# Kernel optimization log

Hardware: AMD Instinct MI355X
Metric: run time of the kernel (lower is better)

The kernel has to match this reference:

```python
import jax, jax.numpy as jnp
import numpy as np

TAU = 0.07          # softmax temperature
THR = 0.3           # Jaccard similarity threshold for positive pairs
EPS_NORM = 1e-12    # F.normalize eps


def setup_inputs() -> dict:
    key = jax.random.key(0)
    k1, k2, k3 = jax.random.split(key, 3)
    N, D, A = 4096, 128, 512
    z1 = jax.random.normal(k1, (N, D), dtype=jnp.float32)
    z2 = jax.random.normal(k2, (N, D), dtype=jnp.float32)
    labels = jax.random.randint(k3, (N, A), 0, 2).astype(jnp.int32)
    return {"z1": z1, "z2": z2, "labels": labels}


def _l2_normalize(x):
    n = jnp.linalg.norm(x, axis=-1, keepdims=True)
    return x / jnp.maximum(n, EPS_NORM)


def reference(z1, z2, labels):
    # Implements the N > 1000 (chunked) branch of SupConLoss.forward,
    # vectorized over all anchors at once (chunking is just tiling; math identical).
    N = z1.shape[0]
    idx = jnp.arange(N)

    z1n = _l2_normalize(z1)                       # (N, D)
    z2n = _l2_normalize(z2)                       # (N, D)
    z_all = jnp.concatenate([z1n, z2n], axis=0)   # (2N, D)

    # Jaccard label similarity -> positive-pair mask
    lab = labels.astype(jnp.float32)              # (N, A)
    inter = lab @ lab.T                           # (N, N)
    s = lab.sum(axis=1, keepdims=True)            # (N, 1)
    union = s + s.T - inter
    jaccard = inter / (union + 1e-8)
    pos_label = jaccard >= THR                    # (N, N) bool

    # pos mask over 2N columns: label-positives in both halves,
    # augmented view [j, N+j] forced True, self column [j, j] forced False.
    pos_mask = jnp.concatenate([pos_label, pos_label], axis=1)  # (N, 2N)
    pos_mask = pos_mask.at[idx, N + idx].set(True)
    pos_mask = pos_mask.at[idx, idx].set(False)

    # similarity of z1 anchors against all 2N embeddings
    sim = (z1n @ z_all.T) / TAU                   # (N, 2N)
    sim = sim - jax.lax.stop_gradient(sim.max(axis=1, keepdims=True))
    exp_sim = jnp.exp(sim)

    # denominator excludes the self column [j, j]
    denom = exp_sim.sum(axis=1, keepdims=True) - exp_sim[idx, idx][:, None]
    log_prob = sim - jnp.log(denom + 1e-8)

    num_pos = jnp.maximum(pos_mask.sum(axis=1), 1)
    loss_per_sample = -jnp.where(pos_mask, log_prob, 0.0).sum(axis=1) / num_pos
    return loss_per_sample.sum() / N
```

## Files before the change

kernel.cpp:

```cpp
#include <hip/hip_runtime.h>
#include <math.h>

#define N_ROWS 4096
#define DIM    128
#define A_LAB  512
#define INV_TAU 14.285714285714286f
#define C_EXP   20.609929155556620f

typedef __attribute__((ext_vector_type(8))) short short8;
typedef __attribute__((ext_vector_type(4))) float f32x4;
typedef __attribute__((ext_vector_type(4))) int i32x4;
typedef __attribute__((ext_vector_type(16))) int i32x16;


__device__ __forceinline__ unsigned short f2bf(float f) {
  unsigned int u = __builtin_bit_cast(unsigned int, f);
  u += 0x7fffu + ((u >> 16) & 1u);
  return (unsigned short)(u >> 16);
}

__global__ __launch_bounds__(256) void k_norm_pack(
    const float* __restrict__ z1, const float* __restrict__ z2,
    const int* __restrict__ labels,
    unsigned int* __restrict__ zbf, uint2* __restrict__ labs8,
    int* __restrict__ s, float* __restrict__ part, float* __restrict__ out)
{
  {
    const int idx = blockIdx.x * 256 + threadIdx.x;
    if (idx < 3 * 4096) part[idx] = 0.0f;
    if (idx == 0) out[0] = 0.0f;
  }
  const int wave = threadIdx.x >> 6, lane = threadIdx.x & 63;
  const int r = blockIdx.x * 4 + wave;
  const float* src = (r < N_ROWS) ? (z1 + (size_t)r * DIM)
                                  : (z2 + (size_t)(r - N_ROWS) * DIM);
  float2 x = ((const float2*)src)[lane];
  float ss = x.x * x.x + x.y * x.y;
  #pragma unroll
  for (int off = 32; off > 0; off >>= 1) ss += __shfl_xor(ss, off);
  const float inv = 1.0f / fmaxf(sqrtf(ss), 1e-12f);
  const unsigned int lo = f2bf(x.x * inv);
  const unsigned int hi = f2bf(x.y * inv);
  {
    const int u = lane >> 2, p = lane & 3;
    const int kf = u >> 2, quad = u & 3;
    const int g = r >> 4;
    zbf[(size_t)(((g * 4 + kf) * 64) + ((r & 15) + (quad << 4))) * 4 + p] = (hi << 16) | lo;
  }

  if (r < N_ROWS) {
    const int4* lp = (const int4*)(labels + (size_t)r * A_LAB);
    const int4 a = lp[2 * lane], b = lp[2 * lane + 1];
    const unsigned int w0 = (unsigned int)(a.x != 0)       | ((unsigned int)(a.y != 0) << 8)
                          | ((unsigned int)(a.z != 0) << 16) | ((unsigned int)(a.w != 0) << 24);
    const unsigned int w1 = (unsigned int)(b.x != 0)       | ((unsigned int)(b.y != 0) << 8)
                          | ((unsigned int)(b.z != 0) << 16) | ((unsigned int)(b.w != 0) << 24);
    uint2 v; v.x = w0; v.y = w1;
    const int ul = lane >> 1, hp = lane & 1;
    const int ks = ul >> 1, h = ul & 1;
    const int g = r >> 5;
    labs8[(size_t)(((g * 16 + ks) * 64) + ((r & 31) + (h << 5))) * 2 + hp] = v;
    int cnt = __popc(w0) + __popc(w1);
    #pragma unroll
    for (int off = 32; off > 0; off >>= 1) cnt += __shfl_xor(cnt, off);
    if (lane == 0) s[r] = cnt;
  }
}

__global__ __launch_bounds__(512, 2) void k_fused(
    const unsigned char* __restrict__ labs8, const int* __restrict__ s,
    const unsigned short* __restrict__ zbf, float* __restrict__ part)
{
  __shared__ unsigned int pmL[128 * 4];
  const int tid = threadIdx.x;
  const int ibase = blockIdx.x * 128, jbase = blockIdx.y * 128;
  const int wave = tid >> 6, lane = tid & 63;
  const bool diag = (ibase == jbase);
  const char* gl = (const char*)labs8;
  const char* gz = (const char*)zbf;

  const int jwr = (wave >> 2) * 64;
  const int jwc = (wave & 3) * 32;
  const int col32 = lane & 31, h = lane >> 5;

  const int s3i = 3 * s[ibase + jwr + lane];
  const int s3j = 3 * s[jbase + jwc + col32];

  i32x16 jacc[2];
  #pragma unroll
  for (int rt = 0; rt < 2; ++rt)
    #pragma unroll
    for (int e = 0; e < 16; ++e) jacc[rt][e] = 0;

  const int gI = (ibase + jwr) >> 5;
  const int gJ = (jbase + jwc) >> 5;
  #pragma unroll
  for (int batch = 0; batch < 2; ++batch) {
    i32x4 av[8][2], bv[8];
    #pragma unroll
    for (int k = 0; k < 8; ++k) {
      const int ks = batch * 8 + k;
      av[k][0] = *(const i32x4*)(gl + (size_t)((gI * 16 + ks) * 64 + lane) * 16);
      av[k][1] = *(const i32x4*)(gl + (size_t)(((gI + 1) * 16 + ks) * 64 + lane) * 16);
      bv[k]    = *(const i32x4*)(gl + (size_t)((gJ * 16 + ks) * 64 + lane) * 16);
    }
    #pragma unroll
    for (int k = 0; k < 8; ++k) {
      jacc[0] = __builtin_amdgcn_mfma_i32_32x32x32_i8(av[k][0], bv[k], jacc[0], 0, 0, 0);
      jacc[1] = __builtin_amdgcn_mfma_i32_32x32x32_i8(av[k][1], bv[k], jacc[1], 0, 0, 0);
    }
  }

  const int wl = wave & 3;
  #pragma unroll
  for (int rt = 0; rt < 2; ++rt)
    #pragma unroll
    for (int reg = 0; reg < 16; ++reg) {
      const int r0 = (reg & 3) + 8 * (reg >> 2);
      const int si = __shfl(s3i, rt * 32 + r0 + 4 * h);
      const bool pred = 13 * jacc[rt][reg] >= si + s3j;
      const unsigned long long bal = __ballot(pred);
      const int lr = jwr + rt * 32 + r0;
      if (lane == 0)      pmL[lr * 4 + wl]       = (unsigned int)bal;
      else if (lane == 1) pmL[(lr + 4) * 4 + wl] = (unsigned int)(bal >> 32);
    }

  const int col = lane & 15, quad = lane >> 4;
  const int srow = wave * 16;
  const int gA = (ibase + srow) >> 4;
  short8 afr[4];
  #pragma unroll
  for (int kf = 0; kf < 4; ++kf)
    afr[kf] = *(const short8*)(gz + (size_t)((gA * 4 + kf) * 64 + lane) * 16);

  __syncthreads();

  uint4 pw[4];
  #pragma unroll
  for (int reg = 0; reg < 4; ++reg)
    pw[reg] = *(const uint4*)&pmL[(srow + quad * 4 + reg) * 4];

  float lacc[4], Sacc[4], Pcnt[4];
  #pragma unroll
  for (int reg = 0; reg < 4; ++reg) { lacc[reg] = 0; Sacc[reg] = 0; Pcnt[reg] = 0; }

  #pragma unroll
  for (int half = 0; half < 2; ++half) {
    const int gB = ((half ? N_ROWS : 0) + jbase) >> 4;
    f32x4 acc[8];
    #pragma unroll
    for (int nt = 0; nt < 8; ++nt) acc[nt] = (f32x4){0, 0, 0, 0};

    #pragma unroll
    for (int batch = 0; batch < 2; ++batch) {
      short8 bv[4][4];
      #pragma unroll
      for (int q = 0; q < 4; ++q) {
        const int nt = batch * 4 + q;
        #pragma unroll
        for (int kf = 0; kf < 4; ++kf)
          bv[q][kf] = *(const short8*)(gz + (size_t)(((gB + nt) * 4 + kf) * 64 + lane) * 16);
      }
      #pragma unroll
      for (int q = 0; q < 4; ++q) {
        const int nt = batch * 4 + q;
        #pragma unroll
        for (int kf = 0; kf < 4; ++kf)
          acc[nt] = __builtin_amdgcn_mfma_f32_16x16x32_bf16(afr[kf], bv[q][kf], acc[nt], 0, 0, 0);
      }
    }

    if (!diag) {
      #pragma unroll
      for (int nt = 0; nt < 8; ++nt) {
        const int bitpos = (nt & 1) * 16 + col;
        #pragma unroll
        for (int reg = 0; reg < 4; ++reg) {
          const unsigned int w = ((const unsigned int*)&pw[reg])[nt >> 1];
          const float d = acc[nt][reg];
          lacc[reg] += exp2f(fmaf(d, C_EXP, -C_EXP));
          if ((w >> bitpos) & 1) Sacc[reg] += d;
        }
      }
    } else {
      const bool left = (half == 0);
      #pragma unroll
      for (int nt = 0; nt < 8; ++nt) {
        const int joff = nt * 16 + col;
        const int jc = jbase + joff;
        const int bitpos = joff & 31;
        #pragma unroll
        for (int reg = 0; reg < 4; ++reg) {
          const int i = ibase + srow + quad * 4 + reg;
          const unsigned int w = ((const unsigned int*)&pw[reg])[nt >> 1];
          const float d = acc[nt][reg];
          const bool bit = (w >> bitpos) & 1;
          const bool self = left && (jc == i);
          const bool pos = left ? (bit && !self) : (bit || (jc == i));
          const float e = exp2f(fmaf(d, C_EXP, -C_EXP));
          if (!self) lacc[reg] += e;
          if (pos) { Sacc[reg] += d; Pcnt[reg] += 1.0f; }
        }
      }
    }
  }

  #pragma unroll
  for (int reg = 0; reg < 4; ++reg) {
    float l = lacc[reg], S = Sacc[reg], P = Pcnt[reg];
    #pragma unroll
    for (int m = 1; m < 16; m <<= 1) {
      l += __shfl_xor(l, m);
      S += __shfl_xor(S, m);
      if (diag) P += __shfl_xor(P, m);
    }
    if (col == 0) {
      const int li = srow + quad * 4 + reg;
      const int i = ibase + li;
      if (!diag) {
        const uint4 w = pw[reg];
        P = 2.0f * (float)(__popc(w.x) + __popc(w.y) + __popc(w.z) + __popc(w.w));
      }
      atomicAdd(&part[i], l);
      atomicAdd(&part[4096 + i], S);
      atomicAdd(&part[8192 + i], P);
    }
  }
}

__global__ __launch_bounds__(128) void k_loss(
    const float* __restrict__ part, float* __restrict__ out)
{
  const int a = blockIdx.x * 128 + threadIdx.x;
  const float l = part[a];
  const float S = part[4096 + a];
  const float P = part[8192 + a];
  const float np = fmaxf(P, 1.0f);
  float v = INV_TAU + logf(l + 1e-8f) - (S * INV_TAU) / np;
  #pragma unroll
  for (int off = 32; off > 0; off >>= 1) v += __shfl_xor(v, off);
  __shared__ float ws2[2];
  const int wave = threadIdx.x >> 6, lane = threadIdx.x & 63;
  if (lane == 0) ws2[wave] = v;
  __syncthreads();
  if (threadIdx.x == 0) atomicAdd(out, (ws2[0] + ws2[1]) * (1.0f / (float)N_ROWS));
}

extern "C" void kernel_launch(void* const* d_in, const int* in_sizes, int n_in,
                              void* d_out, int out_size, void* d_ws, size_t ws_size,
                              hipStream_t stream) {
  const float* z1 = (const float*)d_in[0];
  const float* z2 = (const float*)d_in[1];
  const int* labels = (const int*)d_in[2];
  float* out = (float*)d_out;
  char* ws = (char*)d_ws;

  unsigned int* zbf    = (unsigned int*)(ws);
  uint2* labs8         = (uint2*)(ws + 2097152);
  int* s               = (int*)(ws + 4194304);
  float* part          = (float*)(ws + 4210688);

  hipLaunchKernelGGL(k_norm_pack, dim3(2048), dim3(256), 0, stream,
                     z1, z2, labels, zbf, labs8, s, part, out);
  hipLaunchKernelGGL(k_fused, dim3(32, 32), dim3(512), 0, stream,
                     (const unsigned char*)labs8, s, (const unsigned short*)zbf, part);
  hipLaunchKernelGGL(k_loss, dim3(32), dim3(128), 0, stream, part, out);
}
```

Before: 108.5 us.

## Exploit symmetry of label and z1 Gram matrices with upper-triangular block grid

The fused kernel now launches only the upper-triangular 528 blocks instead of the full 32x32 grid. The label Jaccard mask and the z1·z1 similarity block are computed once per off-diagonal pair and applied to both row i and row j through column-wise reductions. The z1·z2 tiles for both directions are still computed separately. This roughly halves the Jaccard popcount work and one GEMM half per pair, at the cost of more atomics, a triangular index decode loop, and per-block imbalance.

```diff
diff --git a/kernel.cpp b/kernel.cpp
--- a/kernel.cpp
+++ b/kernel.cpp
@@ -73,9 +73,12 @@
 {
   __shared__ unsigned int pmL[128 * 4];
   const int tid = threadIdx.x;
-  const int ibase = blockIdx.x * 128, jbase = blockIdx.y * 128;
+  int t = blockIdx.x, bi = 0;
+  while (t >= 32 - bi) { t -= 32 - bi; ++bi; }
+  const int bj = bi + t;
+  const int ibase = bi * 128, jbase = bj * 128;
   const int wave = tid >> 6, lane = tid & 63;
-  const bool diag = (ibase == jbase);
+  const bool diag = (bi == bj);
   const char* gl = (const char*)labs8;
   const char* gz = (const char*)zbf;
 
@@ -140,49 +143,35 @@
   for (int reg = 0; reg < 4; ++reg)
     pw[reg] = *(const uint4*)&pmL[(srow + quad * 4 + reg) * 4];
 
-  float lacc[4], Sacc[4], Pcnt[4];
-  #pragma unroll
-  for (int reg = 0; reg < 4; ++reg) { lacc[reg] = 0; Sacc[reg] = 0; Pcnt[reg] = 0; }
-
-  #pragma unroll
-  for (int half = 0; half < 2; ++half) {
-    const int gB = ((half ? N_ROWS : 0) + jbase) >> 4;
-    f32x4 acc[8];
-    #pragma unroll
-    for (int nt = 0; nt < 8; ++nt) acc[nt] = (f32x4){0, 0, 0, 0};
-
-    #pragma unroll
-    for (int batch = 0; batch < 2; ++batch) {
-      short8 bv[4][4];
-      #pragma unroll
-      for (int q = 0; q < 4; ++q) {
-        const int nt = batch * 4 + q;
-        #pragma unroll
-        for (int kf = 0; kf < 4; ++kf)
-          bv[q][kf] = *(const short8*)(gz + (size_t)(((gB + nt) * 4 + kf) * 64 + lane) * 16);
-      }
-      #pragma unroll
-      for (int q = 0; q < 4; ++q) {
-        const int nt = batch * 4 + q;
-        #pragma unroll
-        for (int kf = 0; kf < 4; ++kf)
-          acc[nt] = __builtin_amdgcn_mfma_f32_16x16x32_bf16(afr[kf], bv[q][kf], acc[nt], 0, 0, 0);
-      }
-    }
-
-    if (!diag) {
-      #pragma unroll
-      for (int nt = 0; nt < 8; ++nt) {
-        const int bitpos = (nt & 1) * 16 + col;
-        #pragma unroll
-        for (int reg = 0; reg < 4; ++reg) {
-          const unsigned int w = ((const unsigned int*)&pw[reg])[nt >> 1];
-          const float d = acc[nt][reg];
-          lacc[reg] += exp2f(fmaf(d, C_EXP, -C_EXP));
-          if ((w >> bitpos) & 1) Sacc[reg] += d;
-        }
-      }
-    } else {
+  if (diag) {
+    float lacc[4], Sacc[4], Pcnt[4];
+    #pragma unroll
+    for (int reg = 0; reg < 4; ++reg) { lacc[reg] = 0; Sacc[reg] = 0; Pcnt[reg] = 0; }
+
+    #pragma unroll
+    for (int half = 0; half < 2; ++half) {
+      const int gB = ((half ? N_ROWS : 0) + jbase) >> 4;
+      f32x4 acc[8];
+      #pragma unroll
+      for (int nt = 0; nt < 8; ++nt) acc[nt] = (f32x4){0, 0, 0, 0};
+      #pragma unroll
+      for (int batch = 0; batch < 2; ++batch) {
+        short8 bv[4][4];
+        #pragma unroll
+        for (int q = 0; q < 4; ++q) {
+          const int nt = batch * 4 + q;
+          #pragma unroll
+          for (int kf = 0; kf < 4; ++kf)
+            bv[q][kf] = *(const short8*)(gz + (size_t)(((gB + nt) * 4 + kf) * 64 + lane) * 16);
+        }
+        #pragma unroll
+        for (int q = 0; q < 4; ++q) {
+          const int nt = batch * 4 + q;
+          #pragma unroll
+          for (int kf = 0; kf < 4; ++kf)
+            acc[nt] = __builtin_amdgcn_mfma_f32_16x16x32_bf16(afr[kf], bv[q][kf], acc[nt], 0, 0, 0);
+        }
+      }
       const bool left = (half == 0);
       #pragma unroll
       for (int nt = 0; nt < 8; ++nt) {
@@ -203,27 +192,184 @@
         }
       }
     }
-  }
-
-  #pragma unroll
-  for (int reg = 0; reg < 4; ++reg) {
-    float l = lacc[reg], S = Sacc[reg], P = Pcnt[reg];
-    #pragma unroll
-    for (int m = 1; m < 16; m <<= 1) {
-      l += __shfl_xor(l, m);
-      S += __shfl_xor(S, m);
-      if (diag) P += __shfl_xor(P, m);
-    }
-    if (col == 0) {
-      const int li = srow + quad * 4 + reg;
-      const int i = ibase + li;
-      if (!diag) {
-        const uint4 w = pw[reg];
-        P = 2.0f * (float)(__popc(w.x) + __popc(w.y) + __popc(w.z) + __popc(w.w));
-      }
-      atomicAdd(&part[i], l);
-      atomicAdd(&part[4096 + i], S);
-      atomicAdd(&part[8192 + i], P);
+    #pragma unroll
+    for (int reg = 0; reg < 4; ++reg) {
+      float l = lacc[reg], S = Sacc[reg], P = Pcnt[reg];
+      #pragma unroll
+      for (int m = 1; m < 16; m <<= 1) {
+        l += __shfl_xor(l, m);
+        S += __shfl_xor(S, m);
+        P += __shfl_xor(P, m);
+      }
+      if (col == 0) {
+        const int i = ibase + srow + quad * 4 + reg;
+        atomicAdd(&part[i], l);
+        atomicAdd(&part[4096 + i], S);
+        atomicAdd(&part[8192 + i], P);
+      }
+    }
+  } else {
+    float lacc[4], Sacc[4];
+    #pragma unroll
+    for (int reg = 0; reg < 4; ++reg) { lacc[reg] = 0; Sacc[reg] = 0; }
+
+    {
+      const int gB = jbase >> 4;
+      f32x4 acc[8];
+      #pragma unroll
+      for (int nt = 0; nt < 8; ++nt) acc[nt] = (f32x4){0, 0, 0, 0};
+      #pragma unroll
+      for (int batch = 0; batch < 2; ++batch) {
+        short8 bv[4][4];
+        #pragma unroll
+        for (int q = 0; q < 4; ++q) {
+          const int nt = batch * 4 + q;
+          #pragma unroll
+          for (int kf = 0; kf < 4; ++kf)
+            bv[q][kf] = *(const short8*)(gz + (size_t)(((gB + nt) * 4 + kf) * 64 + lane) * 16);
+        }
+        #pragma unroll
+        for (int q = 0; q < 4; ++q) {
+          const int nt = batch * 4 + q;
+          #pragma unroll
+          for (int kf = 0; kf < 4; ++kf)
+            acc[nt] = __builtin_amdgcn_mfma_f32_16x16x32_bf16(afr[kf], bv[q][kf], acc[nt], 0, 0, 0);
+        }
+      }
+      float lc[8], Sc[8], Pc[8];
+      #pragma unroll
+      for (int nt = 0; nt < 8; ++nt) { lc[nt] = 0; Sc[nt] = 0; Pc[nt] = 0; }
+      #pragma unroll
+      for (int nt = 0; nt < 8; ++nt) {
+        const int bitpos = (nt & 1) * 16 + col;
+        #pragma unroll
+        for (int reg = 0; reg < 4; ++reg) {
+          const unsigned int w = ((const unsigned int*)&pw[reg])[nt >> 1];
+          const float d = acc[nt][reg];
+          const bool bit = (w >> bitpos) & 1;
+          const float e = exp2f(fmaf(d, C_EXP, -C_EXP));
+          lacc[reg] += e; lc[nt] += e;
+          if (bit) { Sacc[reg] += d; Sc[nt] += d; Pc[nt] += 1.0f; }
+        }
+      }
+      #pragma unroll
+      for (int nt = 0; nt < 8; ++nt) {
+        float l = lc[nt], S = Sc[nt], P = Pc[nt];
+        l += __shfl_xor(l, 16); l += __shfl_xor(l, 32);
+        S += __shfl_xor(S, 16); S += __shfl_xor(S, 32);
+        P += __shfl_xor(P, 16); P += __shfl_xor(P, 32);
+        if (quad == 0) {
+          const int j = jbase + nt * 16 + col;
+          atomicAdd(&part[j], l);
+          atomicAdd(&part[4096 + j], S);
+          atomicAdd(&part[8192 + j], 2.0f * P);
+        }
+      }
+    }
+
+    {
+      const int gB = (N_ROWS + jbase) >> 4;
+      f32x4 acc[8];
+      #pragma unroll
+      for (int nt = 0; nt < 8; ++nt) acc[nt] = (f32x4){0, 0, 0, 0};
+      #pragma unroll
+      for (int batch = 0; batch < 2; ++batch) {
+        short8 bv[4][4];
+        #pragma unroll
+        for (int q = 0; q < 4; ++q) {
+          const int nt = batch * 4 + q;
+          #pragma unroll
+          for (int kf = 0; kf < 4; ++kf)
+            bv[q][kf] = *(const short8*)(gz + (size_t)(((gB + nt) * 4 + kf) * 64 + lane) * 16);
+        }
+        #pragma unroll
+        for (int q = 0; q < 4; ++q) {
+          const int nt = batch * 4 + q;
+          #pragma unroll
+          for (int kf = 0; kf < 4; ++kf)
+            acc[nt] = __builtin_amdgcn_mfma_f32_16x16x32_bf16(afr[kf], bv[q][kf], acc[nt], 0, 0, 0);
+        }
+      }
+      #pragma unroll
+      for (int nt = 0; nt < 8; ++nt) {
+        const int bitpos = (nt & 1) * 16 + col;
+        #pragma unroll
+        for (int reg = 0; reg < 4; ++reg) {
+          const unsigned int w = ((const unsigned int*)&pw[reg])[nt >> 1];
+          const float d = acc[nt][reg];
+          lacc[reg] += exp2f(fmaf(d, C_EXP, -C_EXP));
+          if ((w >> bitpos) & 1) Sacc[reg] += d;
+        }
+      }
+      #pragma unroll
+      for (int reg = 0; reg < 4; ++reg) {
+        float l = lacc[reg], S = Sacc[reg];
+        #pragma unroll
+        for (int m = 1; m < 16; m <<= 1) { l += __shfl_xor(l, m); S += __shfl_xor(S, m); }
+        if (col == 0) {
+          const int i = ibase + srow + quad * 4 + reg;
+          const uint4 w = pw[reg];
+          const float P = 2.0f * (float)(__popc(w.x) + __popc(w.y) + __popc(w.z) + __popc(w.w));
+          atomicAdd(&part[i], l);
+          atomicAdd(&part[4096 + i], S);
+          atomicAdd(&part[8192 + i], P);
+        }
+      }
+    }
+
+    {
+      const int gA2 = (jbase + srow) >> 4;
+      short8 afr2[4];
+      #pragma unroll
+      for (int kf = 0; kf < 4; ++kf)
+        afr2[kf] = *(const short8*)(gz + (size_t)((gA2 * 4 + kf) * 64 + lane) * 16);
+      const int gB2 = (N_ROWS + ibase) >> 4;
+      f32x4 acc[8];
+      #pragma unroll
+      for (int nt = 0; nt < 8; ++nt) acc[nt] = (f32x4){0, 0, 0, 0};
+      #pragma unroll
+      for (int batch = 0; batch < 2; ++batch) {
+        short8 bv[4][4];
+        #pragma unroll
+        for (int q = 0; q < 4; ++q) {
+          const int nt = batch * 4 + q;
+          #pragma unroll
+          for (int kf = 0; kf < 4; ++kf)
+            bv[q][kf] = *(const short8*)(gz + (size_t)(((gB2 + nt) * 4 + kf) * 64 + lane) * 16);
+        }
+        #pragma unroll
+        for (int q = 0; q < 4; ++q) {
+          const int nt = batch * 4 + q;
+          #pragma unroll
+          for (int kf = 0; kf < 4; ++kf)
+            acc[nt] = __builtin_amdgcn_mfma_f32_16x16x32_bf16(afr2[kf], bv[q][kf], acc[nt], 0, 0, 0);
+        }
+      }
+      float l2[4], S2[4];
+      #pragma unroll
+      for (int reg = 0; reg < 4; ++reg) { l2[reg] = 0; S2[reg] = 0; }
+      const int bp0 = (wave & 1) * 16 + quad * 4;
+      #pragma unroll
+      for (int nt = 0; nt < 8; ++nt) {
+        const unsigned int mw = pmL[(nt * 16 + col) * 4 + (wave >> 1)];
+        #pragma unroll
+        for (int reg = 0; reg < 4; ++reg) {
+          const float d = acc[nt][reg];
+          l2[reg] += exp2f(fmaf(d, C_EXP, -C_EXP));
+          if ((mw >> (bp0 + reg)) & 1) S2[reg] += d;
+        }
+      }
+      #pragma unroll
+      for (int reg = 0; reg < 4; ++reg) {
+        float l = l2[reg], S = S2[reg];
+        #pragma unroll
+        for (int m = 1; m < 16; m <<= 1) { l += __shfl_xor(l, m); S += __shfl_xor(S, m); }
+        if (col == 0) {
+          const int i = jbase + srow + quad * 4 + reg;
+          atomicAdd(&part[i], l);
+          atomicAdd(&part[4096 + i], S);
+        }
+      }
     }
   }
 }
@@ -262,7 +408,7 @@
 
   hipLaunchKernelGGL(k_norm_pack, dim3(2048), dim3(256), 0, stream,
                      z1, z2, labels, zbf, labs8, s, part, out);
-  hipLaunchKernelGGL(k_fused, dim3(32, 32), dim3(512), 0, stream,
+  hipLaunchKernelGGL(k_fused, dim3(528), dim3(512), 0, stream,
                      (const unsigned char*)labs8, s, (const unsigned short*)zbf, part);
   hipLaunchKernelGGL(k_loss, dim3(32), dim3(128), 0, stream, part, out);
 }
```

New measurement: 126.9 us. 1.17x slower.
